# Performance work log

Hardware: AMD Instinct MI355X
Metric: run time of the kernel (lower is better)

## Reference

```python
import jax, jax.numpy as jnp
import numpy as np

N_NODES = 50000
N_EDGES = 1600000
D_NODE = 64
D_EDGE = 64
D_GLOBAL = 32
D_IN = D_EDGE + 2 * D_NODE + D_GLOBAL  # 224


def setup_inputs() -> dict:
    key = jax.random.key(0)
    k = jax.random.split(key, 6)
    edges = jax.random.normal(k[0], (N_EDGES, D_EDGE), dtype=jnp.float32)
    nodes = jax.random.normal(k[1], (N_NODES, D_NODE), dtype=jnp.float32)
    globals_vec = jax.random.normal(k[2], (1, D_GLOBAL), dtype=jnp.float32)
    receivers = jax.random.randint(k[3], (N_EDGES,), 0, N_NODES, dtype=jnp.int64)
    senders = jax.random.randint(k[4], (N_EDGES,), 0, N_NODES, dtype=jnp.int64)
    W = jax.random.normal(k[5], (D_IN, D_EDGE), dtype=jnp.float32) * (1.0 / np.sqrt(D_IN))
    b = jnp.zeros((D_EDGE,), dtype=jnp.float32)
    return {"edges": edges, "nodes": nodes, "globals_vec": globals_vec,
            "receivers": receivers, "senders": senders, "W": W, "b": b}


def reference(edges, nodes, globals_vec, receivers, senders, W, b):
    # gather receiver/sender node features: [E, d_node]
    recv_feat = nodes[receivers]
    send_feat = nodes[senders]
    # broadcast globals to every edge: [E, d_global]
    glob_feat = jnp.broadcast_to(globals_vec, (edges.shape[0], globals_vec.shape[-1]))
    # concat along features, then linear: [E, d_in] @ [d_in, d_edge] + [d_edge]
    collected = jnp.concatenate([edges, recv_feat, send_feat, glob_feat], axis=1)
    updated_edges = collected @ W + b
    return updated_edges
```

## Files before the change

### kernel.cpp

```cpp
#include <hip/hip_runtime.h>

typedef __attribute__((ext_vector_type(8))) short short8;
typedef __attribute__((ext_vector_type(4))) float floatx4;

#define D_NODE 64
#define D_OUT  64

static __device__ __forceinline__ unsigned short f2bf(float x) {
    unsigned int u = __float_as_uint(x);
    unsigned int r = u + 0x7FFFu + ((u >> 16) & 1u);
    return (unsigned short)(r >> 16);
}

static __device__ __forceinline__ short8 cvt2(floatx4 x, floatx4 y) {
    short8 a;
    a[0] = (short)f2bf(x[0]); a[1] = (short)f2bf(x[1]);
    a[2] = (short)f2bf(x[2]); a[3] = (short)f2bf(x[3]);
    a[4] = (short)f2bf(y[0]); a[5] = (short)f2bf(y[1]);
    a[6] = (short)f2bf(y[2]); a[7] = (short)f2bf(y[3]);
    return a;
}

static __device__ __forceinline__ short8 load_cvt(const float* __restrict__ p) {
    return cvt2(*(const floatx4*)p, *(const floatx4*)(p + 4));
}

static __device__ __forceinline__ floatx4 ntload4(const float* __restrict__ p) {
    return __builtin_nontemporal_load((const floatx4*)p);
}

static __device__ __forceinline__ int sz(int r, int ch) {
    return (r << 8) + (((ch << 4)) ^ ((r & 7) << 4));
}

__global__ void pack2_kernel(const float* __restrict__ W, const float* __restrict__ b,
                             const float* __restrict__ g,
                             unsigned short* __restrict__ wpe,
                             unsigned short* __restrict__ wpn,
                             float* __restrict__ gc) {
    int tid = blockIdx.x * 256 + threadIdx.x;
    if (tid < 512) {
        int lane = tid & 63;
        int ct = (tid >> 6) & 3;
        int kstep = tid >> 8;
        int kbase = kstep * 32 + (lane >> 4) * 8;
        int col = 4 * (lane & 15) + ct;
        short8 sv;
#pragma unroll
        for (int j = 0; j < 8; ++j)
            sv[j] = (short)f2bf(W[(size_t)(kbase + j) * D_OUT + col]);
        *(short8*)(wpe + (size_t)tid * 8) = sv;
    } else if (tid < 512 + 1024) {
        int t = tid - 512;
        int lane = t & 63;
        int ct = (t >> 6) & 7;
        int kstep = t >> 9;
        int kk = kstep * 32 + (lane >> 4) * 8;
        int seg = (ct < 4) ? 64 : 128;
        int col = 4 * (lane & 15) + (ct & 3);
        short8 sv;
#pragma unroll
        for (int j = 0; j < 8; ++j)
            sv[j] = (short)f2bf(W[(size_t)(seg + kk + j) * D_OUT + col]);
        *(short8*)(wpn + (size_t)t * 8) = sv;
    } else if (tid < 512 + 1024 + 64) {
        int col = tid - 1536;
        float acc = b[col];
#pragma unroll
        for (int k = 0; k < 32; ++k)
            acc += g[k] * W[(size_t)(192 + k) * D_OUT + col];
        gc[col] = acc;
    }
}

__global__ __launch_bounds__(256) void node3_kernel(
    const float* __restrict__ nodes, const unsigned short* __restrict__ wpn,
    unsigned short* __restrict__ NCb, int Nn) {
    const int lane = threadIdx.x & 63;
    const int wave = threadIdx.x >> 6;
    const int g = lane >> 4;
    int nbase = blockIdx.x * 64 + wave * 16;
    if (nbase >= Nn) return;

    int na = nbase + (lane & 15);
    bool valid = na < Nn;
    if (!valid) na = Nn - 1;
    const float* pn = nodes + (size_t)na * D_NODE + g * 8;
    short8 N0 = load_cvt(pn);
    short8 N1 = load_cvt(pn + 32);

    floatx4 acc[8];
#pragma unroll
    for (int ct = 0; ct < 8; ++ct) {
        short8 B0 = *(const short8*)(wpn + ((size_t)ct * 64 + lane) * 8);
        short8 B1 = *(const short8*)(wpn + ((size_t)(8 + ct) * 64 + lane) * 8);
        acc[ct] = (floatx4){0.f, 0.f, 0.f, 0.f};
        acc[ct] = __builtin_amdgcn_mfma_f32_16x16x32_bf16(B0, N0, acc[ct], 0, 0, 0);
        acc[ct] = __builtin_amdgcn_mfma_f32_16x16x32_bf16(B1, N1, acc[ct], 0, 0, 0);
    }
    if (valid) {
        unsigned short* pr = NCb + (size_t)na * 128 + 16 * g;
#pragma unroll
        for (int j = 0; j < 4; ++j) {
            unsigned short rv[4], sv[4];
#pragma unroll
            for (int ct = 0; ct < 4; ++ct) { rv[ct] = f2bf(acc[ct][j]); sv[ct] = f2bf(acc[4 + ct][j]); }
            *(uint2*)(pr + 4 * j) = *(uint2*)rv;
            *(uint2*)(pr + 64 + 4 * j) = *(uint2*)sv;
        }
    }
}

struct EdgeRegs { floatx4 e0, e1, e2, e3; };
struct GathRegs { uint2 r0, r1, r2, r3, s0, s1, s2, s3; };
struct IdxRegs  { int r0, r1, r2, r3, s0, s1, s2, s3; };

__global__ __launch_bounds__(256) void edge7_kernel(
    const float* __restrict__ edges,
    const int* __restrict__ recv, const int* __restrict__ send,
    const unsigned short* __restrict__ wpe, const unsigned short* __restrict__ NCb,
    const float* __restrict__ gc, float* __restrict__ out, int E, int T) {

    __shared__ float lds[4][1024];

    const int lane = threadIdx.x & 63;
    const int wave = threadIdx.x >> 6;
    const int g = lane >> 4;
    const int e16 = lane & 15;
    const int c = lane & 15;
    const int lr = lane >> 4;
    const int koff = g * 8;
    const int stride = gridDim.x;
    char* buf = (char*)&lds[wave][0];

    short8 Bf[8];
#pragma unroll
    for (int fi = 0; fi < 8; ++fi)
        Bf[fi] = *(const short8*)(wpe + ((size_t)fi * 64 + lane) * 8);

    const floatx4 gc4 = *(const floatx4*)(gc + 4 * c);

    const int t0 = blockIdx.x;
#define TBASE(k) ((t0 + (k) * stride) * 64 + wave * 16)

    auto load_idx = [&](int b) {
        IdxRegs I;
        int q0 = b + 0 + lr;  q0 = (q0 < E) ? q0 : E - 1;
        int q1 = b + 4 + lr;  q1 = (q1 < E) ? q1 : E - 1;
        int q2 = b + 8 + lr;  q2 = (q2 < E) ? q2 : E - 1;
        int q3 = b + 12 + lr; q3 = (q3 < E) ? q3 : E - 1;
        I.r0 = recv[q0]; I.r1 = recv[q1]; I.r2 = recv[q2]; I.r3 = recv[q3];
        I.s0 = send[q0]; I.s1 = send[q1]; I.s2 = send[q2]; I.s3 = send[q3];
        return I;
    };
    auto load_edges = [&](int b) {
        EdgeRegs Er;
        int er = b + e16; er = (er < E) ? er : E - 1;
        const float* pe = edges + (size_t)er * D_NODE + koff;
        Er.e0 = ntload4(pe);
        Er.e1 = ntload4(pe + 4);
        Er.e2 = ntload4(pe + 32);
        Er.e3 = ntload4(pe + 36);
        return Er;
    };
    auto load_gath = [&](const IdxRegs& I) {
        GathRegs G;
        G.r0 = *(const uint2*)(NCb + (size_t)I.r0 * 128 + 4 * c);
        G.r1 = *(const uint2*)(NCb + (size_t)I.r1 * 128 + 4 * c);
        G.r2 = *(const uint2*)(NCb + (size_t)I.r2 * 128 + 4 * c);
        G.r3 = *(const uint2*)(NCb + (size_t)I.r3 * 128 + 4 * c);
        G.s0 = *(const uint2*)(NCb + (size_t)I.s0 * 128 + 64 + 4 * c);
        G.s1 = *(const uint2*)(NCb + (size_t)I.s1 * 128 + 64 + 4 * c);
        G.s2 = *(const uint2*)(NCb + (size_t)I.s2 * 128 + 64 + 4 * c);
        G.s3 = *(const uint2*)(NCb + (size_t)I.s3 * 128 + 64 + 4 * c);
        return G;
    };
    auto addg = [&](floatx4 v, uint2 r, uint2 s) {
        v[0] += __uint_as_float(r.x << 16) + __uint_as_float(s.x << 16);
        v[1] += __uint_as_float(r.x & 0xFFFF0000u) + __uint_as_float(s.x & 0xFFFF0000u);
        v[2] += __uint_as_float(r.y << 16) + __uint_as_float(s.y << 16);
        v[3] += __uint_as_float(r.y & 0xFFFF0000u) + __uint_as_float(s.y & 0xFFFF0000u);
        return v;
    };

    auto compute_store = [&](int b0, const EdgeRegs& Er, const GathRegs& G) {
        short8 A0 = cvt2(Er.e0, Er.e1);
        short8 A1 = cvt2(Er.e2, Er.e3);

        floatx4 acc0 = {0,0,0,0}, acc1 = {0,0,0,0}, acc2 = {0,0,0,0}, acc3 = {0,0,0,0};
        acc0 = __builtin_amdgcn_mfma_f32_16x16x32_bf16(Bf[0], A0, acc0, 0, 0, 0);
        acc1 = __builtin_amdgcn_mfma_f32_16x16x32_bf16(Bf[1], A0, acc1, 0, 0, 0);
        acc2 = __builtin_amdgcn_mfma_f32_16x16x32_bf16(Bf[2], A0, acc2, 0, 0, 0);
        acc3 = __builtin_amdgcn_mfma_f32_16x16x32_bf16(Bf[3], A0, acc3, 0, 0, 0);
        acc0 = __builtin_amdgcn_mfma_f32_16x16x32_bf16(Bf[4], A1, acc0, 0, 0, 0);
        acc1 = __builtin_amdgcn_mfma_f32_16x16x32_bf16(Bf[5], A1, acc1, 0, 0, 0);
        acc2 = __builtin_amdgcn_mfma_f32_16x16x32_bf16(Bf[6], A1, acc2, 0, 0, 0);
        acc3 = __builtin_amdgcn_mfma_f32_16x16x32_bf16(Bf[7], A1, acc3, 0, 0, 0);

#pragma unroll
        for (int j = 0; j < 4; ++j) {
            floatx4 v = (floatx4){acc0[j], acc1[j], acc2[j], acc3[j]};
            *(floatx4*)(buf + sz(e16, 4 * g + j)) = v;
        }

        {
            floatx4 v0 = *(const floatx4*)(buf + sz(0 + lr, c));
            int row = b0 + 0 + lr;
            v0 = addg(v0 + gc4, G.r0, G.s0);
            if (row < E) *(floatx4*)(out + (size_t)row * D_OUT + 4 * c) = v0;
        }
        {
            floatx4 v1 = *(const floatx4*)(buf + sz(4 + lr, c));
            int row = b0 + 4 + lr;
            v1 = addg(v1 + gc4, G.r1, G.s1);
            if (row < E) *(floatx4*)(out + (size_t)row * D_OUT + 4 * c) = v1;
        }
        {
            floatx4 v2 = *(const floatx4*)(buf + sz(8 + lr, c));
            int row = b0 + 8 + lr;
            v2 = addg(v2 + gc4, G.r2, G.s2);
            if (row < E) *(floatx4*)(out + (size_t)row * D_OUT + 4 * c) = v2;
        }
        {
            floatx4 v3 = *(const floatx4*)(buf + sz(12 + lr, c));
            int row = b0 + 12 + lr;
            v3 = addg(v3 + gc4, G.r3, G.s3);
            if (row < E) *(floatx4*)(out + (size_t)row * D_OUT + 4 * c) = v3;
        }
    };

    IdxRegs I0 = load_idx(TBASE(0));
    IdxRegs In = (T > 1) ? load_idx(TBASE(1)) : I0;
    EdgeRegs Ecur = load_edges(TBASE(0));
    GathRegs Gcur = load_gath(I0);

    for (int k = 0; k < T; ++k) {
        EdgeRegs Enext;
        GathRegs Gnext;
        if (k + 1 < T) {
            Enext = load_edges(TBASE(k + 1));
            Gnext = load_gath(In);
        }
        IdxRegs I2 = In;
        if (k + 2 < T)
            I2 = load_idx(TBASE(k + 2));

        compute_store(TBASE(k), Ecur, Gcur);

        if (k + 1 < T) { Ecur = Enext; Gcur = Gnext; }
        In = I2;
    }
#undef TBASE
}


#define NKSTEP 6
#define NFRAG  (NKSTEP * 4)
#define ITERS 4

__global__ void pack_kernel(const float* __restrict__ W, const float* __restrict__ b,
                            const float* __restrict__ g,
                            unsigned short* __restrict__ wp, float* __restrict__ gc) {
    int tid = blockIdx.x * 256 + threadIdx.x;
    if (tid < NFRAG * 64) {
        int lane = tid & 63;
        int ct = (tid >> 6) & 3;
        int kstep = tid >> 8;
        int kbase = kstep * 32 + (lane >> 4) * 8;
        int col = ct * 16 + (lane & 15);
        short8 sv;
#pragma unroll
        for (int j = 0; j < 8; ++j)
            sv[j] = (short)f2bf(W[(size_t)(kbase + j) * D_OUT + col]);
        *(short8*)(wp + (size_t)tid * 8) = sv;
    } else if (tid < NFRAG * 64 + 64) {
        int col = tid - NFRAG * 64;
        float acc = b[col];
#pragma unroll
        for (int k = 0; k < 32; ++k)
            acc += g[k] * W[(size_t)(192 + k) * D_OUT + col];
        gc[col] = acc;
    }
}

__global__ __launch_bounds__(256) void edge_kernel(
    const float* __restrict__ edges, const float* __restrict__ nodes,
    const int* __restrict__ recv, const int* __restrict__ send,
    const unsigned short* __restrict__ wp, const float* __restrict__ gc,
    float* __restrict__ out, int E) {

    const int lane = threadIdx.x & 63;
    const int wave = threadIdx.x >> 6;

    short8 Bf[NFRAG];
#pragma unroll
    for (int fi = 0; fi < NFRAG; ++fi)
        Bf[fi] = *(const short8*)(wp + ((size_t)fi * 64 + lane) * 8);

    const int colbase = lane & 15;
    float gv[4];
#pragma unroll
    for (int ct = 0; ct < 4; ++ct) gv[ct] = gc[ct * 16 + colbase];

    const int koff = (lane >> 4) * 8;

    for (int it = 0; it < ITERS; ++it) {
        int ebase = (blockIdx.x * ITERS + it) * 64 + wave * 16;
        if (ebase >= E) break;

        int ea = ebase + (lane & 15);
        if (ea >= E) ea = E - 1;
        int ri = recv[ea];
        int si = send[ea];

        const float* pe = edges + (size_t)ea * D_NODE + koff;
        const float* pr = nodes + (size_t)ri * D_NODE + koff;
        const float* ps = nodes + (size_t)si * D_NODE + koff;

        short8 A[NKSTEP];
        A[0] = load_cvt(pe);
        A[1] = load_cvt(pe + 32);
        A[2] = load_cvt(pr);
        A[3] = load_cvt(pr + 32);
        A[4] = load_cvt(ps);
        A[5] = load_cvt(ps + 32);

        floatx4 acc[4];
#pragma unroll
        for (int ct = 0; ct < 4; ++ct)
            acc[ct] = (floatx4){gv[ct], gv[ct], gv[ct], gv[ct]};

#pragma unroll
        for (int ks = 0; ks < NKSTEP; ++ks) {
#pragma unroll
            for (int ct = 0; ct < 4; ++ct)
                acc[ct] = __builtin_amdgcn_mfma_f32_16x16x32_bf16(
                    A[ks], Bf[ks * 4 + ct], acc[ct], 0, 0, 0);
        }

        int crow = ebase + (lane >> 4) * 4;
#pragma unroll
        for (int ct = 0; ct < 4; ++ct) {
#pragma unroll
            for (int r4 = 0; r4 < 4; ++r4) {
                int row = crow + r4;
                if (row < E)
                    out[(size_t)row * D_OUT + ct * 16 + colbase] = acc[ct][r4];
            }
        }
    }
}

extern "C" void kernel_launch(void* const* d_in, const int* in_sizes, int n_in,
                              void* d_out, int out_size, void* d_ws, size_t ws_size,
                              hipStream_t stream) {
    const float* edges = (const float*)d_in[0];
    const float* nodes = (const float*)d_in[1];
    const float* glob  = (const float*)d_in[2];
    const int*   recv  = (const int*)d_in[3];
    const int*   send  = (const int*)d_in[4];
    const float* W     = (const float*)d_in[5];
    const float* b     = (const float*)d_in[6];
    float* out = (float*)d_out;

    int E  = in_sizes[0] / D_NODE;
    int Nn = in_sizes[1] / D_NODE;

    size_t nc_bytes  = (size_t)Nn * 128 * 2;
    size_t wpe_bytes = 512 * 8 * 2;
    size_t wpn_bytes = 1024 * 8 * 2;
    size_t need = nc_bytes + wpe_bytes + wpn_bytes + 256;

    if (ws_size >= need) {
        unsigned short* NCb = (unsigned short*)d_ws;
        unsigned short* wpe = (unsigned short*)((char*)d_ws + nc_bytes);
        unsigned short* wpn = (unsigned short*)((char*)d_ws + nc_bytes + wpe_bytes);
        float* gc = (float*)((char*)d_ws + nc_bytes + wpe_bytes + wpn_bytes);

        pack2_kernel<<<7, 256, 0, stream>>>(W, b, glob, wpe, wpn, gc);
        node3_kernel<<<(Nn + 63) / 64, 256, 0, stream>>>(nodes, wpn, NCb, Nn);

        int NT = (E + 63) / 64;
        int grid = (NT < 2500) ? NT : 2500;
        int T = (NT + grid - 1) / grid;
        edge7_kernel<<<grid, 256, 0, stream>>>(edges, recv, send, wpe, NCb, gc, out, E, T);
    } else {
        unsigned short* wp = (unsigned short*)d_ws;
        float* gc = (float*)((char*)d_ws + NFRAG * 64 * 8 * 2);
        pack_kernel<<<7, 256, 0, stream>>>(W, b, glob, wp, gc);
        int nblk = (E + ITERS * 64 - 1) / (ITERS * 64);
        edge_kernel<<<nblk, 256, 0, stream>>>(edges, nodes, recv, send, wp, gc, out, E);
    }
}
```

Baseline: 206.6 us.

## Load edge rows coalesced and stage through double-buffered swizzled LDS

Edge loads change from per-lane strided fragments (8 floats at two offsets per lane) to fully coalesced row-contiguous 16-byte loads. Each tile is written into an XOR-swizzled LDS buffer and read back in MFMA operand layout, double-buffered per wave so staging the next tile overlaps with computing the current one. Output stores become nontemporal. This adds LDS traffic and doubles LDS use per block, which may lower occupancy.

```diff
diff --git a/kernel.cpp b/kernel.cpp
--- a/kernel.cpp
+++ b/kernel.cpp
@@ -27,10 +27,6 @@
 
 static __device__ __forceinline__ floatx4 ntload4(const float* __restrict__ p) {
     return __builtin_nontemporal_load((const floatx4*)p);
-}
-
-static __device__ __forceinline__ int sz(int r, int ch) {
-    return (r << 8) + (((ch << 4)) ^ ((r & 7) << 4));
 }
 
 __global__ void pack2_kernel(const float* __restrict__ W, const float* __restrict__ b,
@@ -111,17 +107,17 @@
     }
 }
 
-struct EdgeRegs { floatx4 e0, e1, e2, e3; };
+struct EdgeRegs { floatx4 v0, v1, v2, v3; };
 struct GathRegs { uint2 r0, r1, r2, r3, s0, s1, s2, s3; };
 struct IdxRegs  { int r0, r1, r2, r3, s0, s1, s2, s3; };
 
-__global__ __launch_bounds__(256) void edge7_kernel(
+__global__ __launch_bounds__(256) void edge8_kernel(
     const float* __restrict__ edges,
     const int* __restrict__ recv, const int* __restrict__ send,
     const unsigned short* __restrict__ wpe, const unsigned short* __restrict__ NCb,
     const float* __restrict__ gc, float* __restrict__ out, int E, int T) {
 
-    __shared__ float lds[4][1024];
+    __shared__ char lds[4][2][4096];
 
     const int lane = threadIdx.x & 63;
     const int wave = threadIdx.x >> 6;
@@ -129,9 +125,8 @@
     const int e16 = lane & 15;
     const int c = lane & 15;
     const int lr = lane >> 4;
-    const int koff = g * 8;
     const int stride = gridDim.x;
-    char* buf = (char*)&lds[wave][0];
+    const int t0 = blockIdx.x;
 
     short8 Bf[8];
 #pragma unroll
@@ -140,7 +135,6 @@
 
     const floatx4 gc4 = *(const floatx4*)(gc + 4 * c);
 
-    const int t0 = blockIdx.x;
 #define TBASE(k) ((t0 + (k) * stride) * 64 + wave * 16)
 
     auto load_idx = [&](int b) {
@@ -155,13 +149,24 @@
     };
     auto load_edges = [&](int b) {
         EdgeRegs Er;
-        int er = b + e16; er = (er < E) ? er : E - 1;
-        const float* pe = edges + (size_t)er * D_NODE + koff;
-        Er.e0 = ntload4(pe);
-        Er.e1 = ntload4(pe + 4);
-        Er.e2 = ntload4(pe + 32);
-        Er.e3 = ntload4(pe + 36);
+#pragma unroll
+        for (int i = 0; i < 4; ++i) {
+            int ci = i * 64 + lane;
+            int row = b + (ci >> 4);
+            row = (row < E) ? row : E - 1;
+            int gch = (ci & 15) ^ ((ci >> 4) & 7);
+            const float* p = edges + (size_t)row * D_NODE + gch * 4;
+            floatx4 v = ntload4(p);
+            if (i == 0) Er.v0 = v; else if (i == 1) Er.v1 = v;
+            else if (i == 2) Er.v2 = v; else Er.v3 = v;
+        }
         return Er;
+    };
+    auto stage_edges = [&](char* buf, const EdgeRegs& Er) {
+        *(floatx4*)(buf + (0 * 64 + lane) * 16) = Er.v0;
+        *(floatx4*)(buf + (1 * 64 + lane) * 16) = Er.v1;
+        *(floatx4*)(buf + (2 * 64 + lane) * 16) = Er.v2;
+        *(floatx4*)(buf + (3 * 64 + lane) * 16) = Er.v3;
     };
     auto load_gath = [&](const IdxRegs& I) {
         GathRegs G;
@@ -183,9 +188,14 @@
         return v;
     };
 
-    auto compute_store = [&](int b0, const EdgeRegs& Er, const GathRegs& G) {
-        short8 A0 = cvt2(Er.e0, Er.e1);
-        short8 A1 = cvt2(Er.e2, Er.e3);
+    auto compute_store = [&](char* buf, int b0, const GathRegs& G) {
+        const int s = (e16 & 7);
+        floatx4 a0lo = *(const floatx4*)(buf + e16 * 256 + ((2 * g + 0) ^ s) * 16);
+        floatx4 a0hi = *(const floatx4*)(buf + e16 * 256 + ((2 * g + 1) ^ s) * 16);
+        floatx4 a1lo = *(const floatx4*)(buf + e16 * 256 + ((2 * g + 8) ^ s) * 16);
+        floatx4 a1hi = *(const floatx4*)(buf + e16 * 256 + ((2 * g + 9) ^ s) * 16);
+        short8 A0 = cvt2(a0lo, a0hi);
+        short8 A1 = cvt2(a1lo, a1hi);
 
         floatx4 acc0 = {0,0,0,0}, acc1 = {0,0,0,0}, acc2 = {0,0,0,0}, acc3 = {0,0,0,0};
         acc0 = __builtin_amdgcn_mfma_f32_16x16x32_bf16(Bf[0], A0, acc0, 0, 0, 0);
@@ -200,55 +210,50 @@
 #pragma unroll
         for (int j = 0; j < 4; ++j) {
             floatx4 v = (floatx4){acc0[j], acc1[j], acc2[j], acc3[j]};
-            *(floatx4*)(buf + sz(e16, 4 * g + j)) = v;
-        }
-
-        {
-            floatx4 v0 = *(const floatx4*)(buf + sz(0 + lr, c));
-            int row = b0 + 0 + lr;
-            v0 = addg(v0 + gc4, G.r0, G.s0);
-            if (row < E) *(floatx4*)(out + (size_t)row * D_OUT + 4 * c) = v0;
-        }
-        {
-            floatx4 v1 = *(const floatx4*)(buf + sz(4 + lr, c));
-            int row = b0 + 4 + lr;
-            v1 = addg(v1 + gc4, G.r1, G.s1);
-            if (row < E) *(floatx4*)(out + (size_t)row * D_OUT + 4 * c) = v1;
-        }
-        {
-            floatx4 v2 = *(const floatx4*)(buf + sz(8 + lr, c));
-            int row = b0 + 8 + lr;
-            v2 = addg(v2 + gc4, G.r2, G.s2);
-            if (row < E) *(floatx4*)(out + (size_t)row * D_OUT + 4 * c) = v2;
-        }
-        {
-            floatx4 v3 = *(const floatx4*)(buf + sz(12 + lr, c));
-            int row = b0 + 12 + lr;
-            v3 = addg(v3 + gc4, G.r3, G.s3);
-            if (row < E) *(floatx4*)(out + (size_t)row * D_OUT + 4 * c) = v3;
+            *(floatx4*)(buf + e16 * 256 + ((4 * g + j) ^ s) * 16) = v;
+        }
+
+#pragma unroll
+        for (int i = 0; i < 4; ++i) {
+            int r = 4 * i + lr;
+            floatx4 v = *(const floatx4*)(buf + r * 256 + (c ^ (r & 7)) * 16);
+            v += gc4;
+            if (i == 0) v = addg(v, G.r0, G.s0);
+            else if (i == 1) v = addg(v, G.r1, G.s1);
+            else if (i == 2) v = addg(v, G.r2, G.s2);
+            else v = addg(v, G.r3, G.s3);
+            int row = b0 + r;
+            if (row < E)
+                __builtin_nontemporal_store(v, (floatx4*)(out + (size_t)row * D_OUT + 4 * c));
         }
     };
 
     IdxRegs I0 = load_idx(TBASE(0));
     IdxRegs In = (T > 1) ? load_idx(TBASE(1)) : I0;
-    EdgeRegs Ecur = load_edges(TBASE(0));
+    {
+        EdgeRegs E0 = load_edges(TBASE(0));
+        stage_edges(&lds[wave][0][0], E0);
+    }
     GathRegs Gcur = load_gath(I0);
-
+    int cur = 0;
+
+#pragma unroll 1
     for (int k = 0; k < T; ++k) {
-        EdgeRegs Enext;
+        const bool more = (k + 1 < T);
+        EdgeRegs Ern;
         GathRegs Gnext;
-        if (k + 1 < T) {
-            Enext = load_edges(TBASE(k + 1));
+        if (more) {
+            Ern = load_edges(TBASE(k + 1));
             Gnext = load_gath(In);
         }
         IdxRegs I2 = In;
-        if (k + 2 < T)
-            I2 = load_idx(TBASE(k + 2));
-
-        compute_store(TBASE(k), Ecur, Gcur);
-
-        if (k + 1 < T) { Ecur = Enext; Gcur = Gnext; }
-        In = I2;
+        if (k + 2 < T) I2 = load_idx(TBASE(k + 2));
+
+        compute_store(&lds[wave][cur][0], TBASE(k), Gcur);
+
+        if (more) stage_edges(&lds[wave][cur ^ 1][0], Ern);
+
+        Gcur = Gnext; In = I2; cur ^= 1;
     }
 #undef TBASE
 }
@@ -383,7 +388,7 @@
         int NT = (E + 63) / 64;
         int grid = (NT < 2500) ? NT : 2500;
         int T = (NT + grid - 1) / grid;
-        edge7_kernel<<<grid, 256, 0, stream>>>(edges, recv, send, wpe, NCb, gc, out, E, T);
+        edge8_kernel<<<grid, 256, 0, stream>>>(edges, recv, send, wpe, NCb, gc, out, E, T);
     } else {
         unsigned short* wp = (unsigned short*)d_ws;
         float* gc = (float*)((char*)d_ws + NFRAG * 64 * 8 * 2);
```

New measurement: 196.3 us. 1.05x faster.
